# Optimization experiments

Measured on AMD Instinct MI355X. Metric: run time of the kernel, lower is better.

The kernel has to match this reference:

```python
import jax, jax.numpy as jnp
import numpy as np
from jax import lax

H = 8          # num_heads
STATE = 16     # SSM state_dim
EPS = 1e-5


def layer_norm(x, g, b):
    mu = jnp.mean(x, axis=-1, keepdims=True)
    var = jnp.mean((x - mu) ** 2, axis=-1, keepdims=True)
    return (x - mu) / jnp.sqrt(var + EPS) * g + b


def linear(x, w, b):
    # torch nn.Linear convention: w [out,in]
    return x @ w.T + b


def cross_attn(q_in, kv_in, qw, qb, kw, kb, vw, vb, ow, ob, g, beta):
    B, Lq, D = q_in.shape
    Lk = kv_in.shape[1]
    hd = D // H
    Q = linear(q_in, qw, qb).reshape(B, Lq, H, hd).transpose(0, 2, 1, 3)
    K = linear(kv_in, kw, kb).reshape(B, Lk, H, hd).transpose(0, 2, 1, 3)
    V = linear(kv_in, vw, vb).reshape(B, Lk, H, hd).transpose(0, 2, 1, 3)
    scores = jnp.einsum('bhqd,bhkd->bhqk', Q, K) / (hd ** 0.5)
    w = jax.nn.softmax(scores, axis=-1)
    out = jnp.einsum('bhqk,bhkd->bhqd', w, V)
    out = out.transpose(0, 2, 1, 3).reshape(B, Lq, D)
    out = linear(out, ow, ob)
    out = layer_norm(out + q_in, g, beta)
    return out, w


def ssm(x, in_w, in_b, A, Bm, C, gw, gb, ow, ob):
    B, L, D = x.shape
    xp = linear(x, in_w, in_b)                      # [B,L,2D]
    x_in = xp[..., D:]                              # second chunk
    gate = jax.nn.sigmoid(linear(x, gw, gb))
    x_in = x_in * gate
    def step(h, xt):
        h = h @ A.T + xt @ Bm.T                     # [B,STATE]
        return h, h @ C.T                           # y [B,D]
    h0 = jnp.zeros((B, STATE), dtype=x.dtype)
    _, ys = lax.scan(step, h0, x_in.transpose(1, 0, 2))
    ys = ys.transpose(1, 0, 2)
    return linear(ys, ow, ob)


def mamba_block(x, p, i):
    y = ssm(layer_norm(x, p['m_ln1_g'][i], p['m_ln1_b'][i]),
            p['m_in_w'][i], p['m_in_b'][i], p['m_A'][i], p['m_B'][i], p['m_C'][i],
            p['m_gate_w'][i], p['m_gate_b'][i], p['m_sout_w'][i], p['m_sout_b'][i])
    x = x + y
    h = layer_norm(x, p['m_ln2_g'][i], p['m_ln2_b'][i])
    h = linear(h, p['m_f1_w'][i], p['m_f1_b'][i])
    h = jax.nn.gelu(h, approximate=False)
    h = linear(h, p['m_f2_w'][i], p['m_f2_b'][i])
    return x + h


def setup_inputs() -> dict:
    key = jax.random.key(0)
    ks = iter(jax.random.split(key, 64))
    B, L, D, BD, VD = 1024, 32, 256, 128, 256
    nB = 6
    def rn(shape, s=0.02):
        return jax.random.normal(next(ks), shape, dtype=jnp.float32) * s
    inp = {
        'ble_features': jax.random.normal(next(ks), (B, L, BD), dtype=jnp.float32),
        'visual_features': jax.random.normal(next(ks), (B, L, VD), dtype=jnp.float32),
        # modality projections
        'bp_w': rn((D, BD)), 'bp_b': jnp.zeros(D), 'bp_emb': rn((D,)),
        'bp_g': jnp.ones(D), 'bp_beta': jnp.zeros(D),
        'vp_w': rn((D, VD)), 'vp_b': jnp.zeros(D), 'vp_emb': rn((D,)),
        'vp_g': jnp.ones(D), 'vp_beta': jnp.zeros(D),
        # two cross-attentions stacked on axis 0: [0]=ble->vis, [1]=vis->ble
        'a_qw': rn((2, D, D)), 'a_qb': jnp.zeros((2, D)),
        'a_kw': rn((2, D, D)), 'a_kb': jnp.zeros((2, D)),
        'a_vw': rn((2, D, D)), 'a_vb': jnp.zeros((2, D)),
        'a_ow': rn((2, D, D)), 'a_ob': jnp.zeros((2, D)),
        'a_g': jnp.ones((2, D)), 'a_beta': jnp.zeros((2, D)),
        # 6 mamba blocks stacked on axis 0
        'm_ln1_g': jnp.ones((nB, D)), 'm_ln1_b': jnp.zeros((nB, D)),
        'm_in_w': rn((nB, 2 * D, D)), 'm_in_b': jnp.zeros((nB, 2 * D)),
        'm_A': rn((nB, STATE, STATE)), 'm_B': rn((nB, STATE, D)), 'm_C': rn((nB, D, STATE)),
        'm_gate_w': rn((nB, D, D)), 'm_gate_b': jnp.zeros((nB, D)),
        'm_sout_w': rn((nB, D, D)), 'm_sout_b': jnp.zeros((nB, D)),
        'm_ln2_g': jnp.ones((nB, D)), 'm_ln2_b': jnp.zeros((nB, D)),
        'm_f1_w': rn((nB, 4 * D, D)), 'm_f1_b': jnp.zeros((nB, 4 * D)),
        'm_f2_w': rn((nB, D, 4 * D)), 'm_f2_b': jnp.zeros((nB, D)),
        # final projection
        'fin_g': jnp.ones(D), 'fin_beta': jnp.zeros(D),
        'fin_w': rn((D, D)), 'fin_b': jnp.zeros(D),
    }
    return inp


def reference(ble_features, visual_features,
              bp_w, bp_b, bp_emb, bp_g, bp_beta,
              vp_w, vp_b, vp_emb, vp_g, vp_beta,
              a_qw, a_qb, a_kw, a_kb, a_vw, a_vb, a_ow, a_ob, a_g, a_beta,
              m_ln1_g, m_ln1_b, m_in_w, m_in_b, m_A, m_B, m_C,
              m_gate_w, m_gate_b, m_sout_w, m_sout_b,
              m_ln2_g, m_ln2_b, m_f1_w, m_f1_b, m_f2_w, m_f2_b,
              fin_g, fin_beta, fin_w, fin_b):
    ble = layer_norm(linear(ble_features, bp_w, bp_b) + bp_emb, bp_g, bp_beta)
    vis = layer_norm(linear(visual_features, vp_w, vp_b) + vp_emb, vp_g, vp_beta)
    # seq_len == target_length -> align_sequences is identity
    ble_att, w_b2v = cross_attn(ble, vis, a_qw[0], a_qb[0], a_kw[0], a_kb[0],
                                a_vw[0], a_vb[0], a_ow[0], a_ob[0], a_g[0], a_beta[0])
    vis_att, w_v2b = cross_attn(vis, ble, a_qw[1], a_qb[1], a_kw[1], a_kb[1],
                                a_vw[1], a_vb[1], a_ow[1], a_ob[1], a_g[1], a_beta[1])
    fused = ble_att + vis_att
    p = dict(m_ln1_g=m_ln1_g, m_ln1_b=m_ln1_b, m_in_w=m_in_w, m_in_b=m_in_b,
             m_A=m_A, m_B=m_B, m_C=m_C, m_gate_w=m_gate_w, m_gate_b=m_gate_b,
             m_sout_w=m_sout_w, m_sout_b=m_sout_b, m_ln2_g=m_ln2_g, m_ln2_b=m_ln2_b,
             m_f1_w=m_f1_w, m_f1_b=m_f1_b, m_f2_w=m_f2_w, m_f2_b=m_f2_b)
    for i in range(m_A.shape[0]):
        fused = mamba_block(fused, p, i)
    g = jnp.mean(fused, axis=1)
    g = layer_norm(g, fin_g, fin_beta)
    g = jax.nn.gelu(linear(g, fin_w, fin_b), approximate=False)
    wb = jnp.mean(w_b2v, axis=(1, 2, 3))
    wv = jnp.mean(w_v2b, axis=(1, 2, 3))
    tot = wb + wv + 1e-6
    return (g, wb / tot, wv / tot)
```

## Files before the change

### kernel.cpp

```cpp
#include <hip/hip_runtime.h>
#include <hip/hip_bf16.h>
#include <math.h>

static constexpr int Bsz  = 1024;
static constexpr int Lseq = 32;
static constexpr int Dm   = 256;
static constexpr int NROW = Bsz * Lseq;

typedef __attribute__((ext_vector_type(8))) short bf16x8;
typedef __attribute__((ext_vector_type(4))) float f32x4;

__device__ __forceinline__ float sigm_f(float x) {
    return 1.0f / (1.0f + __expf(-x));
}
__device__ __forceinline__ float gelu_f(float x) {
    const float u = x * (0.7978845608028654f + 0.0356774081f * x * x);
    return x * sigm_f(2.0f * u);
}
__device__ __forceinline__ float b2f(ushort u) {
    union { float f; uint v; } t; t.v = ((uint)u) << 16; return t.f;
}
__device__ __forceinline__ ushort f2b(float f) {
    union { float f; uint v; } t; t.f = f;
    const uint lsb = (t.v >> 16) & 1u;
    t.v += 0x7fffu + lsb;
    return (ushort)(t.v >> 16);
}

#define GLDS(gp, lp) __builtin_amdgcn_global_load_lds( \
    (const __attribute__((address_space(1))) void*)(gp), \
    (__attribute__((address_space(3))) void*)(lp), 16, 0, 0)


template<int ACT, bool OUTBF, int OMAP, int DUAL>
__global__ __launch_bounds__(256)
void mgemm(const ushort* __restrict__ X, const ushort* __restrict__ W,
           const ushort* __restrict__ W2,
           const float* __restrict__ b1, const float* __restrict__ b2,
           float* __restrict__ Cf, ushort* __restrict__ Cb,
           ushort* __restrict__ Cb2, int K, int M)
{
    __shared__ ushort As[8192];
    __shared__ ushort Bs[8192];
    __shared__ ushort Bs2[DUAL ? 8192 : 8];
    const int tid = threadIdx.x;
    const int w = tid >> 6, l = tid & 63;

    int f = blockIdx.y * gridDim.x + blockIdx.x;
    const int nwg = gridDim.x * gridDim.y;
    if ((nwg & 7) == 0) f = (f & 7) * (nwg >> 3) + (f >> 3);
    const int n0 = (f / gridDim.x) << 7;
    const int m0 = (f % gridDim.x) << 7;

    const int ric = l >> 3;
    const int sl  = l & 7;
    const ushort* gAp[4]; const ushort* gBp[4]; const ushort* gCp[DUAL ? 4 : 1];
    ushort* lAp[4]; ushort* lBp[4]; ushort* lCp[DUAL ? 4 : 1];
    #pragma unroll
    for (int c = 0; c < 4; ++c) {
        const int r = ((w << 2) + c) * 8 + ric;
        const int eo = (sl ^ (r & 7)) << 3;
        gAp[c] = X + (size_t)(n0 + r) * K + eo;
        gBp[c] = W + (size_t)(m0 + r) * K + eo;
        lAp[c] = As + (((w << 2) + c) << 9);
        lBp[c] = Bs + (((w << 2) + c) << 9);
        if constexpr (DUAL) {
            gCp[c] = W2 + (size_t)(m0 + r) * K + eo;
            lCp[c] = Bs2 + (((w << 2) + c) << 9);
        }
    }

    const int wr = (w >> 1) & 1, wc = w & 1;
    const int cl = l & 15, kg = l >> 4;
    int aoff[2][4], boff[2][4];
    #pragma unroll
    for (int sub = 0; sub < 2; ++sub) {
        const int s = sub * 4 + kg;
        #pragma unroll
        for (int m = 0; m < 4; ++m) {
            const int r = wr * 64 + m * 16 + cl;
            aoff[sub][m] = r * 64 + ((s ^ (r & 7)) << 3);
        }
        #pragma unroll
        for (int n = 0; n < 4; ++n) {
            const int r = wc * 64 + n * 16 + cl;
            boff[sub][n] = r * 64 + ((s ^ (r & 7)) << 3);
        }
    }

    f32x4 acc[4][4];
    f32x4 acc2[DUAL ? 4 : 1][DUAL ? 4 : 1];
    #pragma unroll
    for (int m = 0; m < 4; ++m)
        #pragma unroll
        for (int n = 0; n < 4; ++n) {
            acc[m][n] = (f32x4){0.f, 0.f, 0.f, 0.f};
            if constexpr (DUAL) acc2[m][n] = (f32x4){0.f, 0.f, 0.f, 0.f};
        }

    for (int kc = 0; kc < K; kc += 64) {
        #pragma unroll
        for (int c = 0; c < 4; ++c) {
            GLDS(gAp[c], lAp[c]); gAp[c] += 64;
            GLDS(gBp[c], lBp[c]); gBp[c] += 64;
            if constexpr (DUAL) { GLDS(gCp[c], lCp[c]); gCp[c] += 64; }
        }
        __syncthreads();
        #pragma unroll
        for (int sub = 0; sub < 2; ++sub) {
            bf16x8 av[4], bv[4];
            #pragma unroll
            for (int m = 0; m < 4; ++m) av[m] = *(const bf16x8*)(As + aoff[sub][m]);
            #pragma unroll
            for (int n = 0; n < 4; ++n) bv[n] = *(const bf16x8*)(Bs + boff[sub][n]);
            #pragma unroll
            for (int m = 0; m < 4; ++m)
                #pragma unroll
                for (int n = 0; n < 4; ++n)
                    acc[m][n] = __builtin_amdgcn_mfma_f32_16x16x32_bf16(
                        av[m], bv[n], acc[m][n], 0, 0, 0);
            if constexpr (DUAL) {
                bf16x8 cv[4];
                #pragma unroll
                for (int n = 0; n < 4; ++n) cv[n] = *(const bf16x8*)(Bs2 + boff[sub][n]);
                #pragma unroll
                for (int m = 0; m < 4; ++m)
                    #pragma unroll
                    for (int n = 0; n < 4; ++n)
                        acc2[m][n] = __builtin_amdgcn_mfma_f32_16x16x32_bf16(
                            av[m], cv[n], acc2[m][n], 0, 0, 0);
            }
        }
        __syncthreads();
    }

    const int colb = m0 + wc * 64 + cl;
    const int rowb = n0 + wr * 64 + (kg << 2);
    float biasA[4], biasB[4];
    #pragma unroll
    for (int n = 0; n < 4; ++n) {
        biasA[n] = (b1 != nullptr) ? b1[colb + n * 16] : 0.0f;
        if constexpr (DUAL) biasB[n] = b2[colb + n * 16];
    }

    if constexpr (OUTBF || DUAL != 0) {
        ushort* Rw = (w == 0) ? As : (w == 1) ? As + 4096
                   : (w == 2) ? Bs : Bs + 4096;
        const int rr = l >> 3, rc8 = (l & 7) << 3;
        const int nout = (DUAL == 2) ? 2 : 1;
        for (int which = 0; which < nout; ++which) {
            #pragma unroll
            for (int m = 0; m < 4; ++m)
                #pragma unroll
                for (int j = 0; j < 4; ++j) {
                    const int lrow = m * 16 + (kg << 2) + j;
                    #pragma unroll
                    for (int n = 0; n < 4; ++n) {
                        float v;
                        if (which == 0) {
                            v = acc[m][n][j] + biasA[n];
                            if constexpr (DUAL == 1)
                                v = sigm_f(v) * (acc2[m][n][j] + biasB[n]);
                            else if (ACT == 1) v = sigm_f(v);
                            else if (ACT == 2) v = gelu_f(v);
                        } else {
                            v = acc2[m][n][j] + biasB[n];
                        }
                        const int lcol = (n << 4) + cl;
                        Rw[lrow * 64 + (lcol ^ (((lrow >> 1) & 7) << 3))] = f2b(v);
                    }
                }
            ushort* dst = (which == 0) ? Cb : Cb2;
            #pragma unroll
            for (int p = 0; p < 8; ++p) {
                const int lrow = (p << 3) + rr;
                const bf16x8 v8 = *(const bf16x8*)(
                    Rw + lrow * 64 + (rc8 ^ (((lrow >> 1) & 7) << 3)));
                const size_t grow = (size_t)(n0 + wr * 64 + lrow);
                const int gcol = m0 + wc * 64 + rc8;
                size_t idx;
                if (OMAP == 1) idx = grow * 2048 + ((size_t)(gcol >> 4) << 6) + (gcol & 15);
                else           idx = grow * (size_t)M + gcol;
                *(bf16x8*)(dst + idx) = v8;
            }
        }
    } else {
        #pragma unroll
        for (int m = 0; m < 4; ++m)
            #pragma unroll
            for (int j = 0; j < 4; ++j) {
                const size_t row = (size_t)(rowb + m * 16 + j);
                #pragma unroll
                for (int n = 0; n < 4; ++n) {
                    float v = acc[m][n][j] + biasA[n];
                    if (ACT == 1) v = sigm_f(v);
                    else if (ACT == 2) v = gelu_f(v);
                    Cf[row * (size_t)M + colb + n * 16] = v;
                }
            }
    }
}

template<bool ADD_E, bool ACC_F, bool WRV, int LNOUT, bool HASB2>
__global__ __launch_bounds__(256)
void growln_k(const ushort* __restrict__ X, const ushort* __restrict__ W,
              const float* __restrict__ b1, const float* __restrict__ b2,
              const ushort* __restrict__ E, const float* __restrict__ g,
              const float* __restrict__ bt, ushort* __restrict__ Fres,
              ushort* __restrict__ Yb, int K)
{
    __shared__ ushort As[32 * 64];
    __shared__ ushort Bs[256 * 64];
    __shared__ float sred[32][2];
    __shared__ float qred[32][2];
    const int tid = threadIdx.x;
    const int w = tid >> 6, l = tid & 63;
    const int n0 = blockIdx.x << 5;
    const int rowg = w >> 1, colg = w & 1;

    const int ric = l >> 3, sl = l & 7;
    const ushort* gB[8]; ushort* lB[8];
    #pragma unroll
    for (int c = 0; c < 8; ++c) {
        const int rB = ((w << 3) + c) * 8 + ric;
        gB[c] = W + (size_t)rB * K + ((sl ^ (rB & 7)) << 3);
        lB[c] = Bs + (((w << 3) + c) << 9);
    }
    const int rA = (w << 3) + ric;
    const ushort* gA = X + (size_t)(n0 + rA) * K + ((sl ^ (rA & 7)) << 3);
    ushort* lA = As + (w << 9);

    const int cl = l & 15, kg = l >> 4;
    const int ar = rowg * 16 + cl;
    int aoff[2], boff[2][8];
    #pragma unroll
    for (int sub = 0; sub < 2; ++sub) {
        const int s = sub * 4 + kg;
        aoff[sub] = ar * 64 + ((s ^ (ar & 7)) << 3);
        #pragma unroll
        for (int n = 0; n < 8; ++n) {
            const int br = colg * 128 + n * 16 + cl;
            boff[sub][n] = br * 64 + ((s ^ (br & 7)) << 3);
        }
    }

    f32x4 acc[8];
    #pragma unroll
    for (int n = 0; n < 8; ++n) acc[n] = (f32x4){0.f, 0.f, 0.f, 0.f};

    for (int kc = 0; kc < K; kc += 64) {
        #pragma unroll
        for (int c = 0; c < 8; ++c) { GLDS(gB[c], lB[c]); gB[c] += 64; }
        GLDS(gA, lA); gA += 64;
        __syncthreads();
        #pragma unroll
        for (int sub = 0; sub < 2; ++sub) {
            const bf16x8 av = *(const bf16x8*)(As + aoff[sub]);
            #pragma unroll
            for (int n = 0; n < 8; ++n) {
                const bf16x8 bv = *(const bf16x8*)(Bs + boff[sub][n]);
                acc[n] = __builtin_amdgcn_mfma_f32_16x16x32_bf16(av, bv, acc[n], 0, 0, 0);
            }
        }
        __syncthreads();
    }

    float bA[8];
    #pragma unroll
    for (int n = 0; n < 8; ++n) {
        const int col = colg * 128 + n * 16 + cl;
        float v = (b1 != nullptr) ? b1[col] : 0.0f;
        if (HASB2) v += b2[col];
        bA[n] = v;
    }
    float gg[8], bb[8];
    if (LNOUT > 0) {
        #pragma unroll
        for (int n = 0; n < 8; ++n) {
            const int col = colg * 128 + n * 16 + cl;
            gg[n] = g[col]; bb[n] = bt[col];
        }
    }

    #pragma unroll
    for (int j = 0; j < 4; ++j) {
        const int lrow = rowg * 16 + (kg << 2) + j;
        const size_t rb = (size_t)(n0 + lrow) << 8;
        float s = 0.0f;
        #pragma unroll
        for (int n = 0; n < 8; ++n) {
            const size_t idx = rb + colg * 128 + n * 16 + cl;
            float x = acc[n][j] + bA[n];
            if (ADD_E) x += b2f(E[idx]);
            if (ACC_F) x += b2f(Fres[idx]);
            acc[n][j] = x; s += x;
        }
        if (WRV) {
            #pragma unroll
            for (int n = 0; n < 8; ++n)
                Fres[rb + colg * 128 + n * 16 + cl] = f2b(acc[n][j]);
        }
        if (LNOUT > 0) {
            #pragma unroll
            for (int o = 1; o < 16; o <<= 1) s += __shfl_xor(s, o);
            if (cl == 0) sred[lrow][colg] = s;
        }
    }
    if (LNOUT > 0) {
        __syncthreads();
        float mu[4];
        #pragma unroll
        for (int j = 0; j < 4; ++j) {
            const int lrow = rowg * 16 + (kg << 2) + j;
            mu[j] = (sred[lrow][0] + sred[lrow][1]) * (1.0f / 256.0f);
            float q = 0.0f;
            #pragma unroll
            for (int n = 0; n < 8; ++n) { const float d = acc[n][j] - mu[j]; q += d * d; }
            #pragma unroll
            for (int o = 1; o < 16; o <<= 1) q += __shfl_xor(q, o);
            if (cl == 0) qred[lrow][colg] = q;
        }
        __syncthreads();
        #pragma unroll
        for (int j = 0; j < 4; ++j) {
            const int lrow = rowg * 16 + (kg << 2) + j;
            const size_t rb = (size_t)(n0 + lrow) << 8;
            const float rstd = rsqrtf((qred[lrow][0] + qred[lrow][1]) * (1.0f / 256.0f) + 1e-5f);
            #pragma unroll
            for (int n = 0; n < 8; ++n) {
                const float y = (acc[n][j] - mu[j]) * rstd * gg[n] + bb[n];
                const size_t idx = rb + colg * 128 + n * 16 + cl;
                if (LNOUT & 1) Yb[idx] = f2b(y);
                if (LNOUT == 2 || LNOUT == 3) Fres[idx] = f2b(y);
                if (LNOUT == 4) Fres[idx] = f2b(b2f(Fres[idx]) + y);
            }
        }
    }
}

__global__ __launch_bounds__(256)
void ln_k(const ushort* __restrict__ X, const float* __restrict__ g,
          const float* __restrict__ bt, ushort* __restrict__ Yb)
{
    const int lane = threadIdx.x & 63;
    const int row  = (blockIdx.x << 2) + (threadIdx.x >> 6);
    const size_t base = (size_t)row * Dm + (lane << 2);
    const ushort4 u = *reinterpret_cast<const ushort4*>(&X[base]);
    const float v0 = b2f(u.x), v1 = b2f(u.y), v2 = b2f(u.z), v3 = b2f(u.w);
    float s = v0 + v1 + v2 + v3;
    #pragma unroll
    for (int o = 1; o < 64; o <<= 1) s += __shfl_xor(s, o);
    const float mu = s * (1.0f / 256.0f);
    const float d0 = v0 - mu, d1 = v1 - mu, d2 = v2 - mu, d3 = v3 - mu;
    float q = d0*d0 + d1*d1 + d2*d2 + d3*d3;
    #pragma unroll
    for (int o = 1; o < 64; o <<= 1) q += __shfl_xor(q, o);
    const float rstd = rsqrtf(q * (1.0f / 256.0f) + 1e-5f);
    const int c = lane << 2;
    const float4 gg = *reinterpret_cast<const float4*>(&g[c]);
    const float4 bb = *reinterpret_cast<const float4*>(&bt[c]);
    ushort4 ub;
    ub.x = f2b(d0*rstd*gg.x + bb.x); ub.y = f2b(d1*rstd*gg.y + bb.y);
    ub.z = f2b(d2*rstd*gg.z + bb.z); ub.w = f2b(d3*rstd*gg.w + bb.w);
    *reinterpret_cast<ushort4*>(&Yb[base]) = ub;
}

__global__ __launch_bounds__(256)
void attn_k(const ushort* __restrict__ Q, const ushort* __restrict__ K,
            const ushort* __restrict__ V, ushort* __restrict__ O)
{
    __shared__ float Qs[32][33], Ks[32][33], Vs[32][33], Ss[32][33];
    const int bh = blockIdx.x;
    const int b = bh >> 3, h = bh & 7;
    const int tid = threadIdx.x;
    const int r  = tid >> 3;
    const int c4 = (tid & 7) << 2;
    const size_t base = ((size_t)b * Lseq + r) * Dm + h * 32 + c4;
    {
        const ushort4 q = *reinterpret_cast<const ushort4*>(&Q[base]);
        Qs[r][c4+0]=b2f(q.x); Qs[r][c4+1]=b2f(q.y); Qs[r][c4+2]=b2f(q.z); Qs[r][c4+3]=b2f(q.w);
        const ushort4 k = *reinterpret_cast<const ushort4*>(&K[base]);
        Ks[r][c4+0]=b2f(k.x); Ks[r][c4+1]=b2f(k.y); Ks[r][c4+2]=b2f(k.z); Ks[r][c4+3]=b2f(k.w);
        const ushort4 v = *reinterpret_cast<const ushort4*>(&V[base]);
        Vs[r][c4+0]=b2f(v.x); Vs[r][c4+1]=b2f(v.y); Vs[r][c4+2]=b2f(v.z); Vs[r][c4+3]=b2f(v.w);
    }
    __syncthreads();
    float sc[4] = {0.f, 0.f, 0.f, 0.f};
    #pragma unroll
    for (int d = 0; d < 32; ++d) {
        const float qv = Qs[r][d];
        #pragma unroll
        for (int j = 0; j < 4; ++j) sc[j] = fmaf(qv, Ks[c4+j][d], sc[j]);
    }
    #pragma unroll
    for (int j = 0; j < 4; ++j) sc[j] *= 0.17677669529663687f;
    float mx = fmaxf(fmaxf(sc[0], sc[1]), fmaxf(sc[2], sc[3]));
    #pragma unroll
    for (int o = 1; o < 8; o <<= 1) mx = fmaxf(mx, __shfl_xor(mx, o));
    float sum = 0.f;
    #pragma unroll
    for (int j = 0; j < 4; ++j) { sc[j] = __expf(sc[j] - mx); sum += sc[j]; }
    #pragma unroll
    for (int o = 1; o < 8; o <<= 1) sum += __shfl_xor(sum, o);
    const float inv = 1.0f / sum;
    #pragma unroll
    for (int j = 0; j < 4; ++j) Ss[r][c4+j] = sc[j] * inv;
    __syncthreads();
    float o4[4] = {0.f, 0.f, 0.f, 0.f};
    #pragma unroll
    for (int k = 0; k < 32; ++k) {
        const float wv = Ss[r][k];
        #pragma unroll
        for (int j = 0; j < 4; ++j) o4[j] = fmaf(wv, Vs[k][c4+j], o4[j]);
    }
    ushort4 ob; ob.x=f2b(o4[0]); ob.y=f2b(o4[1]); ob.z=f2b(o4[2]); ob.w=f2b(o4[3]);
    *reinterpret_cast<ushort4*>(&O[base]) = ob;
}

__global__ __launch_bounds__(256)
void xb_gemm(const ushort* __restrict__ X, const ushort* __restrict__ Bw,
             ushort* __restrict__ XB)
{
    __shared__ ushort As[128 * 32];
    __shared__ ushort Bsf[16 * 256];
    const int tid = threadIdx.x;
    const int w = tid >> 6, l = tid & 63;
    const int n0 = blockIdx.x << 7;
    #pragma unroll
    for (int rep = 0; rep < 2; ++rep) {
        const int u = (rep << 8) + tid;
        const int r = u >> 5;
        const int c8 = (u & 31) << 3;
        const int di = (r * 256 + c8) ^ ((r & 7) << 3);
        *(bf16x8*)(Bsf + di) = *(const bf16x8*)(Bw + r * 256 + c8);
    }
    const int ric = l >> 2, slot = l & 3;
    const int rL0 = (w << 4) + ric, rL1 = rL0 + 64;
    const int sw0 = slot ^ ((rL0 >> 1) & 3), sw1 = slot ^ ((rL1 >> 1) & 3);
    const ushort* gA0 = X + (size_t)(n0 + rL0) * 256 + (sw0 << 3);
    const ushort* gA1 = X + (size_t)(n0 + rL1) * 256 + (sw1 << 3);
    ushort* lA0 = As + (w << 9);
    ushort* lA1 = As + ((w + 4) << 9);
    const int cl = l & 15, kg = l >> 4;
    int aoff[2];
    #pragma unroll
    for (int m = 0; m < 2; ++m) {
        const int r = w * 32 + m * 16 + cl;
        aoff[m] = r * 32 + ((kg ^ ((r >> 1) & 3)) << 3);
    }
    f32x4 acc[2] = {(f32x4){0.f,0.f,0.f,0.f}, (f32x4){0.f,0.f,0.f,0.f}};
    for (int kc = 0; kc < 256; kc += 32) {
        GLDS(gA0, lA0); GLDS(gA1, lA1);
        gA0 += 32; gA1 += 32;
        __syncthreads();
        const bf16x8 av0 = *(const bf16x8*)(As + aoff[0]);
        const bf16x8 av1 = *(const bf16x8*)(As + aoff[1]);
        const int bidx = (cl * 256 + kc + (kg << 3)) ^ ((cl & 7) << 3);
        const bf16x8 bv = *(const bf16x8*)(Bsf + bidx);
        acc[0] = __builtin_amdgcn_mfma_f32_16x16x32_bf16(av0, bv, acc[0], 0, 0, 0);
        acc[1] = __builtin_amdgcn_mfma_f32_16x16x32_bf16(av1, bv, acc[1], 0, 0, 0);
        __syncthreads();
    }
    #pragma unroll
    for (int m = 0; m < 2; ++m)
        #pragma unroll
        for (int j = 0; j < 4; ++j) {
            const int row = n0 + w * 32 + m * 16 + (kg << 2) + j;
            XB[(size_t)row * 16 + cl] = f2b(acc[m][j]);
        }
}

__global__ __launch_bounds__(256)
void powT_k(const float* __restrict__ A_all, ushort* __restrict__ T_all)
{
    __shared__ float P[2][16][16];
    __shared__ float Asm[16][16];
    const int layer = blockIdx.x;
    const float* A = A_all + layer * 256;
    ushort* T = T_all + (size_t)layer * 262144;
    const int tid = threadIdx.x;
    const int i = tid >> 4, j = tid & 15;
    Asm[i][j] = A[tid];
    const bf16x8 z = {0,0,0,0,0,0,0,0};
    for (int u = tid; u < 32768; u += 256)
        *(bf16x8*)(T + (size_t)u * 8) = z;
    P[0][i][j] = (i == j) ? 1.0f : 0.0f;
    __syncthreads();
    for (int k = 0; k < 32; ++k) {
        const float pv = P[k & 1][i][j];
        const ushort pb = f2b(pv);
        for (int tau = 0; tau + k < 32; ++tau)
            T[(size_t)((tau + k) * 16 + i) * 512 + tau * 16 + j] = pb;
        float acc = 0.0f;
        #pragma unroll
        for (int l2 = 0; l2 < 16; ++l2) acc = fmaf(P[k & 1][i][l2], Asm[l2][j], acc);
        P[(k & 1) ^ 1][i][j] = acc;
        __syncthreads();
    }
}

__global__ __launch_bounds__(256)
void zeroH_k(ushort* __restrict__ Hp)
{
    const int i = blockIdx.x * 256 + threadIdx.x;
    const bf16x8 z = {0,0,0,0,0,0,0,0};
    *(bf16x8*)(Hp + (size_t)i * 8) = z;
}

__global__ __launch_bounds__(256)
void wsc_k(const float* __restrict__ sw, const float* __restrict__ Cc,
           ushort* __restrict__ Wp)
{
    const int i = blockIdx.x >> 4;
    const int m = ((blockIdx.x & 15) << 4) + (threadIdx.x >> 4);
    const int s = threadIdx.x & 15;
    const float* swr = sw + ((size_t)i << 16) + (m << 8);
    const float* cc  = Cc + ((size_t)i << 12) + s;
    float acc = 0.0f;
    #pragma unroll 8
    for (int d = 0; d < 256; ++d) acc = fmaf(swr[d], cc[d << 4], acc);
    ushort* o = Wp + ((size_t)i << 14) + (m << 6);
    o[s] = f2b(acc);
    o[s + 16] = 0; o[s + 32] = 0; o[s + 48] = 0;
}

__global__ __launch_bounds__(256)
void meanL_k(const ushort* __restrict__ X, ushort* __restrict__ G)
{
    const int idx = blockIdx.x * 256 + threadIdx.x;
    const int b = idx >> 8, d = idx & 255;
    const ushort* xp = X + (size_t)b * (Lseq * Dm) + d;
    float s = 0.0f;
    #pragma unroll
    for (int t = 0; t < Lseq; ++t) s += b2f(xp[t << 8]);
    G[idx] = f2b(s * (1.0f / 32.0f));
}

__global__ __launch_bounds__(256)
void fillw_k(float* __restrict__ out)
{
    const int i = blockIdx.x * 256 + threadIdx.x;
    const float wm = 1.0f / 32.0f;
    out[i] = wm / (wm + wm + 1e-6f);
}

__global__ __launch_bounds__(256)
void cast_k(const float* __restrict__ src, ushort* __restrict__ dst, int n4)
{
    const int i = blockIdx.x * 256 + threadIdx.x;
    if (i < n4) {
        const float4 v = reinterpret_cast<const float4*>(src)[i];
        ushort4 o; o.x = f2b(v.x); o.y = f2b(v.y); o.z = f2b(v.z); o.w = f2b(v.w);
        reinterpret_cast<ushort4*>(dst)[i] = o;
    }
}

__global__ __launch_bounds__(256)
void cast_inw_k(const float* __restrict__ src, ushort* __restrict__ dst)
{
    const int i = blockIdx.x * 256 + threadIdx.x;
    const int blk = i >> 14, rem = i & 16383;
    const float4 v = reinterpret_cast<const float4*>(
        src + (size_t)blk * 131072 + 65536)[rem];
    ushort4 o; o.x = f2b(v.x); o.y = f2b(v.y); o.z = f2b(v.z); o.w = f2b(v.w);
    reinterpret_cast<ushort4*>(dst)[i] = o;
}

extern "C" void kernel_launch(void* const* d_in, const int* in_sizes, int n_in,
                              void* d_out, int out_size, void* d_ws, size_t ws_size,
                              hipStream_t stream)
{
    const float* ble_f   = (const float*)d_in[0];
    const float* vis_f   = (const float*)d_in[1];
    const float* bp_w    = (const float*)d_in[2];
    const float* bp_b    = (const float*)d_in[3];
    const float* bp_emb  = (const float*)d_in[4];
    const float* bp_g    = (const float*)d_in[5];
    const float* bp_beta = (const float*)d_in[6];
    const float* vp_w    = (const float*)d_in[7];
    const float* vp_b    = (const float*)d_in[8];
    const float* vp_emb  = (const float*)d_in[9];
    const float* vp_g    = (const float*)d_in[10];
    const float* vp_beta = (const float*)d_in[11];
    const float* a_qw    = (const float*)d_in[12];
    const float* a_qb    = (const float*)d_in[13];
    const float* a_kw    = (const float*)d_in[14];
    const float* a_kb    = (const float*)d_in[15];
    const float* a_vw    = (const float*)d_in[16];
    const float* a_vb    = (const float*)d_in[17];
    const float* a_ow    = (const float*)d_in[18];
    const float* a_ob    = (const float*)d_in[19];
    const float* a_g     = (const float*)d_in[20];
    const float* a_beta  = (const float*)d_in[21];
    const float* m_ln1_g = (const float*)d_in[22];
    const float* m_ln1_b = (const float*)d_in[23];
    const float* m_in_w  = (const float*)d_in[24];
    const float* m_in_b  = (const float*)d_in[25];
    const float* m_A     = (const float*)d_in[26];
    const float* m_B     = (const float*)d_in[27];
    const float* m_C     = (const float*)d_in[28];
    const float* m_gw    = (const float*)d_in[29];
    const float* m_gb    = (const float*)d_in[30];
    const float* m_sw    = (const float*)d_in[31];
    const float* m_sb    = (const float*)d_in[32];
    const float* m_ln2_g = (const float*)d_in[33];
    const float* m_ln2_b = (const float*)d_in[34];
    const float* m_f1w   = (const float*)d_in[35];
    const float* m_f1b   = (const float*)d_in[36];
    const float* m_f2w   = (const float*)d_in[37];
    const float* m_f2b   = (const float*)d_in[38];
    const float* fin_g   = (const float*)d_in[39];
    const float* fin_beta= (const float*)d_in[40];
    const float* fin_w   = (const float*)d_in[41];
    const float* fin_b   = (const float*)d_in[42];

    float* out = (float*)d_out;
    float* ws  = (float*)d_ws;
    const size_t NDf = (size_t)NROW * Dm;

    ushort* F_res = (ushort*)ws;
    ushort* Gpool = F_res + NDf;
    float*  F2    = ws + 3 * NDf;
    ushort* S0 = (ushort*)(ws + 4 * NDf);
    ushort* S1 = S0 + NDf;
    ushort* S2 = S1 + NDf;
    ushort* S3 = S2 + NDf;
    ushort* S4 = S3 + NDf;
    ushort* Wa = S4 + NDf;
    ushort* W_bp  = Wa;
    ushort* W_vp  = W_bp + 32768;
    ushort* W_q   = W_vp + 65536;
    ushort* W_k   = W_q + 131072;
    ushort* W_v   = W_k + 131072;
    ushort* W_o   = W_v + 131072;
    ushort* W_g   = W_o + 131072;
    ushort* W_in  = W_g + 393216;
    ushort* W_f1  = W_in + 393216;
    ushort* W_f2  = W_f1 + 1572864;
    ushort* W_fin = W_f2 + 1572864;
    ushort* W_sc  = W_fin + 65536;
    ushort* Hpad  = W_sc + 98304;
    ushort* B_ble = (ushort*)F2;
    ushort* B_vis = B_ble + (size_t)NROW * 128;
    ushort* T_all = (ushort*)F2;
    ushort* W_bm  = T_all + 1572864;
    ushort* XBuf  = W_bm + 24576;

    const dim3 blk(256);
    auto cgrid = [](int n4) { return dim3((n4 + 255) / 256); };

    cast_k<<<cgrid(1048576), blk, 0, stream>>>(ble_f, B_ble, 1048576);
    cast_k<<<cgrid(2097152), blk, 0, stream>>>(vis_f, B_vis, 2097152);
    cast_k<<<cgrid(8192),   blk, 0, stream>>>(bp_w, W_bp, 8192);
    cast_k<<<cgrid(16384),  blk, 0, stream>>>(vp_w, W_vp, 16384);
    cast_k<<<cgrid(32768),  blk, 0, stream>>>(a_qw, W_q, 32768);
    cast_k<<<cgrid(32768),  blk, 0, stream>>>(a_kw, W_k, 32768);
    cast_k<<<cgrid(32768),  blk, 0, stream>>>(a_vw, W_v, 32768);
    cast_k<<<cgrid(32768),  blk, 0, stream>>>(a_ow, W_o, 32768);
    cast_k<<<cgrid(98304),  blk, 0, stream>>>(m_gw, W_g, 98304);
    cast_k<<<cgrid(393216), blk, 0, stream>>>(m_f1w, W_f1, 393216);
    cast_k<<<cgrid(393216), blk, 0, stream>>>(m_f2w, W_f2, 393216);
    cast_k<<<cgrid(16384),  blk, 0, stream>>>(fin_w, W_fin, 16384);
    cast_inw_k<<<cgrid(98304), blk, 0, stream>>>(m_in_w, W_in);
    wsc_k<<<96, blk, 0, stream>>>(m_sw, m_C, W_sc);

    auto gg = [](int M, int N) { return dim3(M / 128, N / 128); };
    const dim3 gRow(NROW / 32);

    growln_k<false,false,false,1,true><<<gRow, blk, 0, stream>>>(
        B_ble, W_bp, bp_b, bp_emb, nullptr, bp_g, bp_beta, nullptr, S0, 128);
    growln_k<false,false,false,1,true><<<gRow, blk, 0, stream>>>(
        B_vis, W_vp, vp_b, vp_emb, nullptr, vp_g, vp_beta, nullptr, S1, 256);

    for (int a = 0; a < 2; ++a) {
        const ushort* qin_b = (a == 0) ? S0 : S1;
        const ushort* kin_b = (a == 0) ? S1 : S0;
        const size_t wo = (size_t)a * 65536;
        const size_t bo = (size_t)a * 256;
        mgemm<0,true,0,0><<<gg(256, NROW), blk, 0, stream>>>(
            qin_b, W_q + wo, nullptr, a_qb + bo, nullptr, nullptr, S4, nullptr, 256, 256);
        mgemm<0,true,0,2><<<gg(256, NROW), blk, 0, stream>>>(
            kin_b, W_k + wo, W_v + wo, a_kb + bo, a_vb + bo, nullptr, S2, S3, 256, 256);
        attn_k<<<Bsz * 8, blk, 0, stream>>>(S4, S2, S3, S4);
        if (a == 0)
            growln_k<true,false,false,2,false><<<gRow, blk, 0, stream>>>(
                S4, W_o + wo, a_ob + bo, nullptr, qin_b, a_g + bo, a_beta + bo, F_res, nullptr, 256);
        else
            growln_k<true,false,false,4,false><<<gRow, blk, 0, stream>>>(
                S4, W_o + wo, a_ob + bo, nullptr, qin_b, a_g + bo, a_beta + bo, F_res, nullptr, 256);
    }

    powT_k<<<6, blk, 0, stream>>>(m_A, T_all);
    cast_k<<<cgrid(6144), blk, 0, stream>>>(m_B, W_bm, 6144);
    zeroH_k<<<1024, blk, 0, stream>>>(Hpad);

    ln_k<<<NROW/4, blk, 0, stream>>>(F_res, m_ln1_g, m_ln1_b, S0);

    for (int i = 0; i < 6; ++i) {
        mgemm<0,true,0,1><<<gg(256, NROW), blk, 0, stream>>>(
            S0, W_g + (size_t)i*65536, W_in + (size_t)i*65536,
            m_gb + i*256, m_in_b + (size_t)i*512 + 256, nullptr, S2, nullptr, 256, 256);
        xb_gemm<<<NROW/128, blk, 0, stream>>>(S2, W_bm + (size_t)i*4096, XBuf);
        mgemm<0,true,1,0><<<gg(512, 1024), blk, 0, stream>>>(
            XBuf, T_all + (size_t)i*262144, nullptr, nullptr, nullptr, nullptr, Hpad, nullptr, 512, 512);
        growln_k<false,true,true,1,false><<<gRow, blk, 0, stream>>>(
            Hpad, W_sc + (size_t)i*16384, m_sb + i*256, nullptr, nullptr,
            m_ln2_g + i*256, m_ln2_b + i*256, F_res, S0, 64);
        mgemm<2,true,0,0><<<gg(1024, NROW), blk, 0, stream>>>(
            S0, W_f1 + (size_t)i*262144, nullptr, m_f1b + i*1024, nullptr, nullptr, S1, nullptr, 256, 1024);
        if (i < 5)
            growln_k<false,true,true,1,false><<<gRow, blk, 0, stream>>>(
                S1, W_f2 + (size_t)i*262144, m_f2b + i*256, nullptr, nullptr,
                m_ln1_g + (i+1)*256, m_ln1_b + (i+1)*256, F_res, S0, 1024);
        else
            growln_k<false,true,true,0,false><<<gRow, blk, 0, stream>>>(
                S1, W_f2 + (size_t)i*262144, m_f2b + i*256, nullptr, nullptr,
                nullptr, nullptr, F_res, nullptr, 1024);
    }

    meanL_k<<<(Bsz * Dm) / 256, blk, 0, stream>>>(F_res, Gpool);
    ln_k<<<Bsz/4, blk, 0, stream>>>(Gpool, fin_g, fin_beta, S1);
    mgemm<2,false,0,0><<<gg(256, Bsz), blk, 0, stream>>>(
        S1, W_fin, nullptr, fin_b, nullptr, out, nullptr, nullptr, 256, 256);
    fillw_k<<<8, blk, 0, stream>>>(out + (size_t)Bsz * Dm);
}
```

Baseline: 1.100 ms.

## Add dedicated 128x256-tile FFN1 GEMM and skip zero blocks in scan GEMM

```diff
diff --git a/kernel.cpp b/kernel.cpp
--- a/kernel.cpp
+++ b/kernel.cpp
@@ -98,7 +98,8 @@
             if constexpr (DUAL) acc2[m][n] = (f32x4){0.f, 0.f, 0.f, 0.f};
         }
 
-    for (int kc = 0; kc < K; kc += 64) {
+    const int Klim = (OMAP == 1) ? (m0 + 128 < K ? m0 + 128 : K) : K;
+    for (int kc = 0; kc < Klim; kc += 64) {
         #pragma unroll
         for (int c = 0; c < 4; ++c) {
             GLDS(gAp[c], lAp[c]); gAp[c] += 64;
@@ -198,6 +199,115 @@
                     Cf[row * (size_t)M + colb + n * 16] = v;
                 }
             }
+    }
+}
+
+__global__ __launch_bounds__(256, 2)
+void f1_gemm(const ushort* __restrict__ X, const ushort* __restrict__ W,
+             const float* __restrict__ b1, ushort* __restrict__ Cb)
+{
+    __shared__ ushort As[8192];
+    __shared__ ushort Bs[16384];
+    const int tid = threadIdx.x;
+    const int w = tid >> 6, l = tid & 63;
+
+    int f = blockIdx.y * 4 + blockIdx.x;
+    f = (f & 7) * 128 + (f >> 3);
+    const int n0 = (f >> 2) << 7;
+    const int m0 = (f & 3) << 8;
+
+    const int ric = l >> 3, sl = l & 7;
+    const ushort* gAp[4]; ushort* lAp[4];
+    const ushort* gBp[8]; ushort* lBp[8];
+    #pragma unroll
+    for (int c = 0; c < 4; ++c) {
+        const int r = ((w << 2) + c) * 8 + ric;
+        gAp[c] = X + (size_t)(n0 + r) * 256 + ((sl ^ (r & 7)) << 3);
+        lAp[c] = As + (((w << 2) + c) << 9);
+    }
+    #pragma unroll
+    for (int c = 0; c < 8; ++c) {
+        const int r = ((w << 3) + c) * 8 + ric;
+        gBp[c] = W + (size_t)(m0 + r) * 256 + ((sl ^ (r & 7)) << 3);
+        lBp[c] = Bs + (((w << 3) + c) << 9);
+    }
+
+    const int wr = (w >> 1) & 1, wc = w & 1;
+    const int cl = l & 15, kg = l >> 4;
+    int aoff[2][4], boff[2][8];
+    #pragma unroll
+    for (int sub = 0; sub < 2; ++sub) {
+        const int s = sub * 4 + kg;
+        #pragma unroll
+        for (int m = 0; m < 4; ++m) {
+            const int r = wr * 64 + m * 16 + cl;
+            aoff[sub][m] = r * 64 + ((s ^ (r & 7)) << 3);
+        }
+        #pragma unroll
+        for (int n = 0; n < 8; ++n) {
+            const int r = wc * 128 + n * 16 + cl;
+            boff[sub][n] = r * 64 + ((s ^ (r & 7)) << 3);
+        }
+    }
+
+    f32x4 acc[4][8];
+    #pragma unroll
+    for (int m = 0; m < 4; ++m)
+        #pragma unroll
+        for (int n = 0; n < 8; ++n) acc[m][n] = (f32x4){0.f, 0.f, 0.f, 0.f};
+
+    for (int kc = 0; kc < 256; kc += 64) {
+        #pragma unroll
+        for (int c = 0; c < 4; ++c) { GLDS(gAp[c], lAp[c]); gAp[c] += 64; }
+        #pragma unroll
+        for (int c = 0; c < 8; ++c) { GLDS(gBp[c], lBp[c]); gBp[c] += 64; }
+        __syncthreads();
+        #pragma unroll
+        for (int sub = 0; sub < 2; ++sub) {
+            bf16x8 av[4], bv[8];
+            #pragma unroll
+            for (int m = 0; m < 4; ++m) av[m] = *(const bf16x8*)(As + aoff[sub][m]);
+            #pragma unroll
+            for (int n = 0; n < 8; ++n) bv[n] = *(const bf16x8*)(Bs + boff[sub][n]);
+            #pragma unroll
+            for (int m = 0; m < 4; ++m)
+                #pragma unroll
+                for (int n = 0; n < 8; ++n)
+                    acc[m][n] = __builtin_amdgcn_mfma_f32_16x16x32_bf16(
+                        av[m], bv[n], acc[m][n], 0, 0, 0);
+        }
+        __syncthreads();
+    }
+
+    float bA[8];
+    #pragma unroll
+    for (int n = 0; n < 8; ++n) bA[n] = b1[m0 + wc * 128 + n * 16 + cl];
+
+    ushort* Rw = Bs + (w << 12);
+    const int rr = l >> 3, rc8 = (l & 7) << 3;
+    #pragma unroll
+    for (int h = 0; h < 2; ++h) {
+        #pragma unroll
+        for (int m = 0; m < 4; ++m)
+            #pragma unroll
+            for (int j = 0; j < 4; ++j) {
+                const int lrow = m * 16 + (kg << 2) + j;
+                #pragma unroll
+                for (int n = 0; n < 4; ++n) {
+                    const float v = gelu_f(acc[m][h * 4 + n][j] + bA[h * 4 + n]);
+                    const int lcol = (n << 4) + cl;
+                    Rw[lrow * 64 + (lcol ^ (((lrow >> 1) & 7) << 3))] = f2b(v);
+                }
+            }
+        #pragma unroll
+        for (int p = 0; p < 8; ++p) {
+            const int lrow = (p << 3) + rr;
+            const bf16x8 v8 = *(const bf16x8*)(
+                Rw + lrow * 64 + (rc8 ^ (((lrow >> 1) & 7) << 3)));
+            const size_t grow = (size_t)(n0 + wr * 64 + lrow);
+            const int gcol = m0 + wc * 128 + h * 64 + rc8;
+            *(bf16x8*)(Cb + grow * 1024 + gcol) = v8;
+        }
     }
 }
 
@@ -706,8 +816,8 @@
         growln_k<false,true,true,1,false><<<gRow, blk, 0, stream>>>(
             Hpad, W_sc + (size_t)i*16384, m_sb + i*256, nullptr, nullptr,
             m_ln2_g + i*256, m_ln2_b + i*256, F_res, S0, 64);
-        mgemm<2,true,0,0><<<gg(1024, NROW), blk, 0, stream>>>(
-            S0, W_f1 + (size_t)i*262144, nullptr, m_f1b + i*1024, nullptr, nullptr, S1, nullptr, 256, 1024);
+        f1_gemm<<<dim3(4, 256), blk, 0, stream>>>(
+            S0, W_f1 + (size_t)i*262144, m_f1b + i*1024, S1);
         if (i < 5)
             growln_k<false,true,true,1,false><<<gRow, blk, 0, stream>>>(
                 S1, W_f2 + (size_t)i*262144, m_f2b + i*256, nullptr, nullptr,
```

New measurement: 1.137 ms. 3.3% more time.
